# Kernel tuning notes

Measured on AMD Instinct MI355X. Metric: run time of the kernel, lower is better.

## Reference

```python
import jax, jax.numpy as jnp
import numpy as np
import math

D_MODEL = 256
NUM_SLOTS = 128
RANK = 32
STEPS = 6
VOCAB = 32000
SEQ = 512
BATCH = 8
LN_EPS = 1e-5


def setup_inputs() -> dict:
    key = jax.random.key(0)
    ks = jax.random.split(key, 16)
    std = 0.02
    inp = {
        "input_ids": jax.random.randint(ks[0], (BATCH, SEQ), 0, VOCAB),
        "attention_mask": jnp.ones((BATCH, SEQ), dtype=jnp.int32),
        "token_emb": jax.random.normal(ks[1], (VOCAB, D_MODEL), jnp.float32) * std,
        "pos_emb": jax.random.normal(ks[2], (SEQ, D_MODEL), jnp.float32) * std,
        "H": jax.random.normal(ks[3], (NUM_SLOTS, D_MODEL), jnp.float32) / math.sqrt(D_MODEL),
        "W_source": jax.random.normal(ks[4], (NUM_SLOTS, NUM_SLOTS, D_MODEL, RANK), jnp.float32) * std,
        "W_target": jax.random.normal(ks[5], (NUM_SLOTS, NUM_SLOTS, RANK, D_MODEL), jnp.float32) * std,
        "Wq_in": jax.random.normal(ks[6], (D_MODEL, D_MODEL), jnp.float32) / math.sqrt(D_MODEL),
        "Wk_slots": jax.random.normal(ks[7], (D_MODEL, D_MODEL), jnp.float32) / math.sqrt(D_MODEL),
        "Wv_in": jax.random.normal(ks[8], (D_MODEL, D_MODEL), jnp.float32) / math.sqrt(D_MODEL),
        "Wq_out": jax.random.normal(ks[9], (D_MODEL, D_MODEL), jnp.float32) / math.sqrt(D_MODEL),
        "Wk_fin": jax.random.normal(ks[10], (D_MODEL, D_MODEL), jnp.float32) / math.sqrt(D_MODEL),
        "Wv_fin": jax.random.normal(ks[11], (D_MODEL, D_MODEL), jnp.float32) / math.sqrt(D_MODEL),
        "W_out_proj": jax.random.normal(ks[12], (VOCAB, D_MODEL), jnp.float32) / math.sqrt(D_MODEL),
        "ln_scale": jnp.ones((STEPS, D_MODEL), jnp.float32),
        "ln_bias": jnp.zeros((STEPS, D_MODEL), jnp.float32),
    }
    return inp


def _layernorm(x, g, b):
    mu = jnp.mean(x, axis=-1, keepdims=True)
    var = jnp.var(x, axis=-1, keepdims=True)
    return (x - mu) / jnp.sqrt(var + LN_EPS) * g + b


def _forward(input_ids, attention_mask, token_emb, pos_emb, H, W_source, W_target,
             Wq_in, Wk_slots, Wv_in, Wq_out, Wk_fin, Wv_fin, W_out_proj, ln_scale, ln_bias):
    B, L = input_ids.shape
    scale = 1.0 / math.sqrt(D_MODEL)
    # embeddings (dropout is identity in eval)
    X = token_emb[input_ids] + pos_emb[jnp.arange(L)][None]  # (B,L,D)
    # compress: input tokens -> slots
    Q_in = X @ Wq_in.T                      # (B,L,D)
    K_sl = H @ Wk_slots.T                   # (S,D)
    V_in = X @ Wv_in.T                      # (B,L,D)
    A = jax.nn.softmax(Q_in @ K_sl.T * scale, axis=-1)  # (B,L,S)
    m = attention_mask.astype(A.dtype)[..., None]
    A = A * m
    A = A / (jnp.sum(A, axis=1, keepdims=True) + 1e-8)
    IR = jnp.einsum('bls,bld->bsd', A, V_in)            # (B,S,D)
    H_state = H[None] + IR                               # (B,S,D)

    off_diag = (1.0 - jnp.eye(NUM_SLOTS, dtype=H_state.dtype))  # (S,S)

    def step(h, lnp):
        g, b = lnp
        # bilinear slot-to-slot influence; contract directly, no (B,S,S,D) expand of h
        inter = jnp.einsum('bid,ijdr->bijr', h, W_source)        # (B,S,S,R)
        out = jnp.einsum('bijr,ijrd->bijd', inter, W_target)     # (B,S,S,D)
        infl = jnp.einsum('bijd,ij->bjd', out, off_diag)         # mask diag + sum over i
        h = _layernorm(h + jax.nn.relu(infl), g, b)
        return h, None

    H_state, _ = jax.lax.scan(step, H_state, (ln_scale, ln_bias))

    # expand: slots -> tokens
    Q_out = X @ Wq_out.T                   # (B,L,D)
    K_f = H_state @ Wk_fin.T               # (B,S,D)
    V_f = H_state @ Wv_fin.T               # (B,S,D)
    A2 = jax.nn.softmax(jnp.einsum('bld,bsd->bls', Q_out, K_f) * scale, axis=-1)
    Y = jnp.einsum('bls,bsd->bld', A2, V_f)
    logits = Y @ W_out_proj.T              # (B,L,V)
    return logits


def reference(input_ids, attention_mask, token_emb, pos_emb, H, W_source, W_target,
              Wq_in, Wk_slots, Wv_in, Wq_out, Wk_fin, Wv_fin, W_out_proj, ln_scale, ln_bias):
    return _forward(input_ids, attention_mask, token_emb, pos_emb, H, W_source, W_target,
                    Wq_in, Wk_slots, Wv_in, Wq_out, Wk_fin, Wv_fin, W_out_proj, ln_scale, ln_bias)
```

## Files before the change

kernel.cpp:

```cpp
#include <hip/hip_runtime.h>
#include <hip/hip_bf16.h>
#include <math.h>

#define D_MODEL 256
#define NUM_SLOTS 128
#define RANK 32
#define N_STEPS 6
#define VOCAB 32000
#define SEQ 512
#define BATCH 8
#define NTOK (BATCH*SEQ)
#define LN_EPS 1e-5f
#define SM_SCALE 0.0625f
#define IGROUPS 8
#define IPG (NUM_SLOTS/IGROUPS)

typedef __attribute__((ext_vector_type(8))) short bf16x8;
typedef __attribute__((ext_vector_type(8))) _Float16 f16x8;
typedef __attribute__((ext_vector_type(4))) float f32x4;

#define GLD_LDS16(g, l) __builtin_amdgcn_global_load_lds( \
    (const __attribute__((address_space(1))) unsigned int*)(g), \
    (__attribute__((address_space(3))) unsigned int*)(l), 16, 0, 0)

__device__ inline unsigned short f2bf(float x) {
    unsigned u = __float_as_uint(x);
    unsigned r = u + 0x7fff + ((u >> 16) & 1);
    return (unsigned short)(r >> 16);
}
__device__ inline float bf2f(unsigned short h) {
    return __uint_as_float(((unsigned)h) << 16);
}
__device__ inline unsigned pk2(float a, float b) {
    auto v = __builtin_amdgcn_cvt_pkrtz(a, b);
    union { decltype(v) x; unsigned u; } c;
    c.x = v;
    return c.u;
}
__device__ inline unsigned short f2h(float x) {
    union { _Float16 h; unsigned short u; } c;
    c.h = (_Float16)x;
    return c.u;
}
__device__ inline float h2f(unsigned short u) {
    union { unsigned short u; _Float16 h; } c;
    c.u = u;
    return (float)c.h;
}

__global__ __launch_bounds__(256) void k_embed(const int* __restrict__ ids,
        const float* __restrict__ tok, const float* __restrict__ pos,
        float* __restrict__ X) {
    int bl = blockIdx.x;
    int d  = threadIdx.x;
    int l  = bl % SEQ;
    int id = ids[bl];
    X[(size_t)bl*D_MODEL + d] = tok[(size_t)id*D_MODEL + d] + pos[l*D_MODEL + d];
}

__global__ __launch_bounds__(256) void k_gemm_nt(const float* __restrict__ A,
        const float* __restrict__ B, float* __restrict__ C, int M, int N, int K) {
    __shared__ float As[32][64];
    __shared__ float Bs[32][64];
    int bm = blockIdx.x * 64, bn = blockIdx.y * 64;
    int t = threadIdx.x;
    int tm = (t & 15) * 4, tn = (t >> 4) * 4;
    float acc[4][4] = {};
    for (int k0 = 0; k0 < K; k0 += 32) {
        #pragma unroll
        for (int r = 0; r < 8; ++r) {
            int idx = r*256 + t;
            int m = idx >> 5, k = idx & 31;
            As[k][m] = A[(size_t)(bm+m)*K + k0 + k];
        }
        #pragma unroll
        for (int r = 0; r < 8; ++r) {
            int idx = r*256 + t;
            int n = idx >> 5, k = idx & 31;
            Bs[k][n] = B[(size_t)(bn+n)*K + k0 + k];
        }
        __syncthreads();
        #pragma unroll
        for (int k = 0; k < 32; ++k) {
            float4 a4 = *(const float4*)&As[k][tm];
            float4 b4 = *(const float4*)&Bs[k][tn];
            float a[4] = {a4.x,a4.y,a4.z,a4.w};
            float b[4] = {b4.x,b4.y,b4.z,b4.w};
            #pragma unroll
            for (int i = 0; i < 4; ++i)
                #pragma unroll
                for (int jj = 0; jj < 4; ++jj)
                    acc[i][jj] += a[i]*b[jj];
        }
        __syncthreads();
    }
    #pragma unroll
    for (int i = 0; i < 4; ++i) {
        float4 v = make_float4(acc[i][0],acc[i][1],acc[i][2],acc[i][3]);
        *(float4*)&C[(size_t)(bm+tm+i)*N + bn+tn] = v;
    }
}

__global__ __launch_bounds__(256) void k_gemm3(const float* __restrict__ A,
        const float* __restrict__ B0, const float* __restrict__ B1,
        const float* __restrict__ B2, float* __restrict__ C0,
        float* __restrict__ C1, float* __restrict__ C2) {
    const int K = D_MODEL, N = D_MODEL;
    const float* B = blockIdx.z == 0 ? B0 : (blockIdx.z == 1 ? B1 : B2);
    float* C = blockIdx.z == 0 ? C0 : (blockIdx.z == 1 ? C1 : C2);
    __shared__ float As[32][64];
    __shared__ float Bs[32][64];
    int bm = blockIdx.x * 64, bn = blockIdx.y * 64;
    int t = threadIdx.x;
    int tm = (t & 15) * 4, tn = (t >> 4) * 4;
    float acc[4][4] = {};
    for (int k0 = 0; k0 < K; k0 += 32) {
        #pragma unroll
        for (int r = 0; r < 8; ++r) {
            int idx = r*256 + t;
            int m = idx >> 5, k = idx & 31;
            As[k][m] = A[(size_t)(bm+m)*K + k0 + k];
        }
        #pragma unroll
        for (int r = 0; r < 8; ++r) {
            int idx = r*256 + t;
            int n = idx >> 5, k = idx & 31;
            Bs[k][n] = B[(size_t)(bn+n)*K + k0 + k];
        }
        __syncthreads();
        #pragma unroll
        for (int k = 0; k < 32; ++k) {
            float4 a4 = *(const float4*)&As[k][tm];
            float4 b4 = *(const float4*)&Bs[k][tn];
            float a[4] = {a4.x,a4.y,a4.z,a4.w};
            float b[4] = {b4.x,b4.y,b4.z,b4.w};
            #pragma unroll
            for (int i = 0; i < 4; ++i)
                #pragma unroll
                for (int jj = 0; jj < 4; ++jj)
                    acc[i][jj] += a[i]*b[jj];
        }
        __syncthreads();
    }
    #pragma unroll
    for (int i = 0; i < 4; ++i) {
        float4 v = make_float4(acc[i][0],acc[i][1],acc[i][2],acc[i][3]);
        *(float4*)&C[(size_t)(bm+tm+i)*N + bn+tn] = v;
    }
}

__global__ __launch_bounds__(256) void k_split16(const float* __restrict__ in,
        unsigned short* __restrict__ o, int n4) {
    int i = blockIdx.x*256 + threadIdx.x;
    if (i >= n4) return;
    float4 v = ((const float4*)in)[i];
    ushort4 h;
    h.x = f2h(v.x); h.y = f2h(v.y); h.z = f2h(v.z); h.w = f2h(v.w);
    ((ushort4*)o)[i] = h;
}

__global__ __launch_bounds__(256) void k_logits(
        const unsigned short* __restrict__ Ahg, const unsigned short* __restrict__ Alg,
        const unsigned short* __restrict__ Bhg, float* __restrict__ C) {
    __shared__ short lds[3*128*64];
    short* Ah = lds;
    short* Al = lds + 8192;
    short* Bh = lds + 16384;
    int bm = blockIdx.x * 128, bn = blockIdx.y * 128;
    int t = threadIdx.x;
    int w = t >> 6, l = t & 63;
    int wr = w >> 1, wc = w & 1;
    int lr = l & 15, lk = l >> 4;
    f32x4 acc[4][4];
    #pragma unroll
    for (int mi = 0; mi < 4; ++mi)
        #pragma unroll
        for (int ni = 0; ni < 4; ++ni)
            acc[mi][ni] = (f32x4){0.f,0.f,0.f,0.f};

    for (int kc = 0; kc < 4; ++kc) {
        #pragma unroll
        for (int i = 0; i < 4; ++i) {
            int v = t + i*256;
            int row = v >> 3, cv = v & 7;
            int so = row*64 + ((cv ^ (row & 7)) << 3);
            size_t ga = (size_t)(bm+row)*256 + kc*64 + cv*8;
            size_t gb = (size_t)(bn+row)*256 + kc*64 + cv*8;
            *(bf16x8*)&Ah[so] = *(const bf16x8*)&Ahg[ga];
            *(bf16x8*)&Al[so] = *(const bf16x8*)&Alg[ga];
            *(bf16x8*)&Bh[so] = *(const bf16x8*)&Bhg[gb];
        }
        __syncthreads();
        #pragma unroll
        for (int s = 0; s < 2; ++s) {
            f16x8 ah[4], al[4], bh[4];
            #pragma unroll
            for (int mi = 0; mi < 4; ++mi) {
                int row = wr*64 + mi*16 + lr;
                int off = row*64 + ((((s<<2)+lk) ^ (row&7)) << 3);
                ah[mi] = *(f16x8*)&Ah[off];
                al[mi] = *(f16x8*)&Al[off];
            }
            #pragma unroll
            for (int ni = 0; ni < 4; ++ni) {
                int row = wc*64 + ni*16 + lr;
                int off = row*64 + ((((s<<2)+lk) ^ (row&7)) << 3);
                bh[ni] = *(f16x8*)&Bh[off];
            }
            #pragma unroll
            for (int mi = 0; mi < 4; ++mi)
                #pragma unroll
                for (int ni = 0; ni < 4; ++ni) {
                    acc[mi][ni] = __builtin_amdgcn_mfma_f32_16x16x32_f16(ah[mi], bh[ni], acc[mi][ni], 0, 0, 0);
                    acc[mi][ni] = __builtin_amdgcn_mfma_f32_16x16x32_f16(al[mi], bh[ni], acc[mi][ni], 0, 0, 0);
                }
        }
        __syncthreads();
    }
    #pragma unroll
    for (int mi = 0; mi < 4; ++mi)
        #pragma unroll
        for (int ni = 0; ni < 4; ++ni) {
            int col = bn + wc*64 + ni*16 + lr;
            #pragma unroll
            for (int r = 0; r < 4; ++r) {
                int row = bm + wr*64 + mi*16 + lk*4 + r;
                C[(size_t)row*VOCAB + col] = acc[mi][ni][r];
            }
        }
}

__global__ __launch_bounds__(128) void k_softmax_mask(float* __restrict__ A,
        const int* __restrict__ mask) {
    int row = blockIdx.x;
    int s = threadIdx.x;
    __shared__ float red[128];
    float v = A[(size_t)row*NUM_SLOTS + s] * SM_SCALE;
    red[s] = v; __syncthreads();
    for (int o = 64; o > 0; o >>= 1) { if (s < o) red[s] = fmaxf(red[s], red[s+o]); __syncthreads(); }
    float mx = red[0]; __syncthreads();
    float e = expf(v - mx);
    red[s] = e; __syncthreads();
    for (int o = 64; o > 0; o >>= 1) { if (s < o) red[s] += red[s+o]; __syncthreads(); }
    float sum = red[0];
    float m = (float)mask[row];
    A[(size_t)row*NUM_SLOTS + s] = e / sum * m;
}

__global__ __launch_bounds__(128) void k_colsum(const float* __restrict__ A,
        float* __restrict__ csp) {
    int b = blockIdx.x; int ch = blockIdx.y; int s = threadIdx.x;
    const float* Ab = A + ((size_t)b*SEQ + ch*64)*NUM_SLOTS + s;
    float a0 = 0.f, a1 = 0.f, a2 = 0.f, a3 = 0.f;
    #pragma unroll
    for (int l = 0; l < 64; l += 4) {
        a0 += Ab[(size_t)(l+0)*NUM_SLOTS];
        a1 += Ab[(size_t)(l+1)*NUM_SLOTS];
        a2 += Ab[(size_t)(l+2)*NUM_SLOTS];
        a3 += Ab[(size_t)(l+3)*NUM_SLOTS];
    }
    csp[(b*8 + ch)*NUM_SLOTS + s] = (a0+a1) + (a2+a3);
}

__global__ __launch_bounds__(256) void k_ir(const float* __restrict__ A,
        const float* __restrict__ V, const float* __restrict__ H,
        const float* __restrict__ csp, float* __restrict__ Hs,
        unsigned short* __restrict__ Hs16) {
    int bs = blockIdx.x; int b = bs >> 7; int s = bs & 127;
    int d = threadIdx.x;
    float sum = 1e-8f;
    #pragma unroll
    for (int p = 0; p < 8; ++p) sum += csp[(b*8 + p)*NUM_SLOTS + s];
    float inv = 1.0f / sum;
    const float* Ab = A + (size_t)b*SEQ*NUM_SLOTS + s;
    const float* Vb = V + (size_t)b*SEQ*D_MODEL + d;
    float a0 = 0.f, a1 = 0.f, a2 = 0.f, a3 = 0.f;
    for (int l = 0; l < SEQ; l += 4) {
        a0 += Ab[(size_t)(l+0)*NUM_SLOTS] * Vb[(size_t)(l+0)*D_MODEL];
        a1 += Ab[(size_t)(l+1)*NUM_SLOTS] * Vb[(size_t)(l+1)*D_MODEL];
        a2 += Ab[(size_t)(l+2)*NUM_SLOTS] * Vb[(size_t)(l+2)*D_MODEL];
        a3 += Ab[(size_t)(l+3)*NUM_SLOTS] * Vb[(size_t)(l+3)*D_MODEL];
    }
    float acc = (a0+a1) + (a2+a3);
    float v = H[s*D_MODEL + d] + acc * inv;
    Hs[(size_t)bs*D_MODEL + d] = v;
    Hs16[(size_t)bs*D_MODEL + d] = f2h(v);
}

__global__ __launch_bounds__(256) void k_convert_s(const float* __restrict__ Ws,
        unsigned short* __restrict__ WF) {
    int i = blockIdx.x, j = blockIdx.y, hf = blockIdx.z;
    int t = threadIdx.x;
    __shared__ float lds[128*33];
    size_t sBase = ((size_t)i*128 + j)*8192;
    size_t pOut = ((size_t)j*128 + i)*16384;
    const float4* s4 = (const float4*)(Ws + sBase) + hf*1024;
    #pragma unroll
    for (int p = 0; p < 4; ++p) {
        int f4 = p*256 + t;
        float4 v = s4[f4];
        *(float4*)&lds[(f4 >> 3)*33 + 4*(f4 & 7)] = v;
    }
    __syncthreads();
    bool diag = (i == j);
    #pragma unroll
    for (int q = 0; q < 2; ++q) {
        int cl = q*256 + t;
        int ksl = cl >> 7, mt = (cl >> 6) & 1, l = cl & 63;
        int g = l >> 4, c = l & 15;
        union { f16x8 v; } o;
        #pragma unroll
        for (int e = 0; e < 8; ++e) {
            float f = diag ? 0.f : lds[(ksl*32 + g*8 + e)*33 + mt*16 + c];
            o.v[e] = (_Float16)f;
        }
        *(f16x8*)(WF + pOut + (size_t)hf*4096 + (size_t)cl*8) = o.v;
    }
}

__global__ __launch_bounds__(256) void k_convert_t(const float* __restrict__ Wt,
        unsigned short* __restrict__ WF) {
    int i = blockIdx.x, j = blockIdx.y, hf = blockIdx.z;
    int t = threadIdx.x;
    __shared__ float lds[32*133];
    size_t sBase = ((size_t)i*128 + j)*8192;
    size_t pOut = ((size_t)j*128 + i)*16384;
    const float4* s4 = (const float4*)(Wt + sBase);
    #pragma unroll
    for (int p = 0; p < 4; ++p) {
        int idx = p*256 + t;
        int r = idx >> 5, c4 = idx & 31;
        float4 v = s4[r*64 + hf*32 + c4];
        *(float4*)&lds[r*133 + c4*4] = v;
    }
    __syncthreads();
    #pragma unroll
    for (int q = 0; q < 2; ++q) {
        int cl = q*256 + t;
        int ntl = cl >> 6, l = cl & 63;
        int g = l >> 4, c = l & 15;
        union { f16x8 v; } o;
        #pragma unroll
        for (int e = 0; e < 8; ++e)
            o.v[e] = (_Float16)lds[(g*8 + e)*133 + ntl*16 + c];
        *(f16x8*)(WF + pOut + 8192 + (size_t)hf*4096 + (size_t)cl*8) = o.v;
    }
}

__global__ __launch_bounds__(256, 4) void k_pairs_mfma(const unsigned short* __restrict__ h16,
        const unsigned short* __restrict__ WF, float* __restrict__ part) {
    __shared__ unsigned short lds[2*10240];
    int j = blockIdx.x, g = blockIdx.y;
    int t = threadIdx.x, w = t >> 6, l = t & 63;
    int lg = l >> 4, c = l & 15;
    const unsigned short* pbase = WF + ((size_t)j*128 + g*16)*16384;

    {
        const unsigned short* src = pbase;
        #pragma unroll
        for (int q = 0; q < 4; ++q)
            GLD_LDS16(src + (size_t)(q*256 + t)*8, &lds[(q*256 + t)*8]);
        const unsigned short* hsrc = h16 + ((size_t)(t&7)*NUM_SLOTS + g*16)*D_MODEL + (t>>3)*8;
        GLD_LDS16(hsrc, &lds[8192 + t*8]);
    }
    __builtin_amdgcn_sched_barrier(0);
    f16x8 bqn[4];
    #pragma unroll
    for (int nt = 0; nt < 4; ++nt)
        bqn[nt] = *(const f16x8*)(pbase + 8192 + (size_t)((w*4+nt)*64 + l)*8);
    __builtin_amdgcn_sched_barrier(0);

    f32x4 acc[4];
    #pragma unroll
    for (int nt = 0; nt < 4; ++nt) acc[nt] = (f32x4){0.f,0.f,0.f,0.f};
    f16x8 hzero;
    #pragma unroll
    for (int e = 0; e < 8; ++e) hzero[e] = (_Float16)0.f;

    #pragma unroll 2
    for (int ii = 0; ii < 16; ++ii) {
        int cur = ii & 1;
        asm volatile("s_waitcnt vmcnt(4) lgkmcnt(0)" ::: "memory");
        __builtin_amdgcn_s_barrier();
        __builtin_amdgcn_sched_barrier(0);
        if (ii < 15) {
            const unsigned short* src = pbase + (size_t)(ii+1)*16384;
            unsigned short* dst = &lds[(cur^1)*10240];
            #pragma unroll
            for (int q = 0; q < 4; ++q)
                GLD_LDS16(src + (size_t)(q*256 + t)*8, dst + (size_t)(q*256 + t)*8);
            const unsigned short* hsrc = h16 + ((size_t)(t&7)*NUM_SLOTS + (g*16+ii+1))*D_MODEL + (t>>3)*8;
            GLD_LDS16(hsrc, dst + 8192 + (size_t)t*8);
        }
        __builtin_amdgcn_sched_barrier(0);
        f16x8 bq[4];
        #pragma unroll
        for (int nt = 0; nt < 4; ++nt) bq[nt] = bqn[nt];
        if (ii < 15) {
            const unsigned short* bp = pbase + (size_t)(ii+1)*16384 + 8192;
            #pragma unroll
            for (int nt = 0; nt < 4; ++nt)
                bqn[nt] = *(const f16x8*)(bp + (size_t)((w*4+nt)*64 + l)*8);
        }
        const unsigned short* buf = &lds[cur*10240];
        f32x4 d1[2];
        d1[0] = (f32x4){0.f,0.f,0.f,0.f};
        d1[1] = (f32x4){0.f,0.f,0.f,0.f};
        #pragma unroll
        for (int ks = 0; ks < 8; ++ks) {
            f16x8 a0 = *(const f16x8*)(buf + (size_t)((ks*2+0)*64 + l)*8);
            f16x8 a1 = *(const f16x8*)(buf + (size_t)((ks*2+1)*64 + l)*8);
            f16x8 hv = *(const f16x8*)(buf + 8192 + (size_t)(((ks*4+lg)*8 + (c&7)))*8);
            f16x8 hb = (c < 8) ? hv : hzero;
            d1[0] = __builtin_amdgcn_mfma_f32_16x16x32_f16(a0, hb, d1[0], 0, 0, 0);
            d1[1] = __builtin_amdgcn_mfma_f32_16x16x32_f16(a1, hb, d1[1], 0, 0, 0);
        }
        unsigned q0 = pk2(d1[0][0], d1[0][1]);
        unsigned q1 = pk2(d1[0][2], d1[0][3]);
        unsigned s0 = pk2(d1[1][0], d1[1][1]);
        unsigned s1 = pk2(d1[1][2], d1[1][3]);
        int srcLo = 32*(lg & 1) + c;
        int srcHi = srcLo + 16;
        unsigned a0s = (unsigned)__shfl((int)q0, srcLo, 64);
        unsigned a1s = (unsigned)__shfl((int)q1, srcLo, 64);
        unsigned a2s = (unsigned)__shfl((int)q0, srcHi, 64);
        unsigned a3s = (unsigned)__shfl((int)q1, srcHi, 64);
        unsigned b0s = (unsigned)__shfl((int)s0, srcLo, 64);
        unsigned b1s = (unsigned)__shfl((int)s1, srcLo, 64);
        unsigned b2s = (unsigned)__shfl((int)s0, srcHi, 64);
        unsigned b3s = (unsigned)__shfl((int)s1, srcHi, 64);
        bool himt = ((lg >> 1) & 1);
        union { unsigned u[4]; f16x8 v; } A2u;
        A2u.u[0] = himt ? b0s : a0s;
        A2u.u[1] = himt ? b1s : a1s;
        A2u.u[2] = himt ? b2s : a2s;
        A2u.u[3] = himt ? b3s : a3s;
        #pragma unroll
        for (int nt = 0; nt < 4; ++nt)
            acc[nt] = __builtin_amdgcn_mfma_f32_16x16x32_f16(A2u.v, bq[nt], acc[nt], 0, 0, 0);
    }
    if (lg < 2) {
        #pragma unroll
        for (int nt = 0; nt < 4; ++nt) {
            int d = (w*4 + nt)*16 + c;
            #pragma unroll
            for (int r = 0; r < 4; ++r) {
                int b = lg*4 + r;
                part[(((size_t)g*BATCH + b)*NUM_SLOTS + j)*D_MODEL + d] = acc[nt][r];
            }
        }
    }
}

__global__ __launch_bounds__(256) void k_pairs(const float* __restrict__ h,
        const float* __restrict__ Ws, const float* __restrict__ Wt,
        float* __restrict__ part) {
    int j = blockIdx.x;
    int g = blockIdx.y;
    int t = threadIdx.x;
    __shared__ float sh_h[BATCH][D_MODEL];
    __shared__ float sh_inter[BATCH][RANK];
    float acc[BATCH];
    #pragma unroll
    for (int b = 0; b < BATCH; ++b) acc[b] = 0.f;
    int tb = t >> 5, tr = t & 31;
    for (int ii = 0; ii < IPG; ++ii) {
        int i = g*IPG + ii;
        if (i == j) continue;
        #pragma unroll
        for (int b = 0; b < BATCH; ++b)
            sh_h[b][t] = h[((size_t)b*NUM_SLOTS + i)*D_MODEL + t];
        __syncthreads();
        const float* ws = Ws + ((size_t)i*NUM_SLOTS + j)*(D_MODEL*RANK);
        float accA = 0.f;
        #pragma unroll 8
        for (int d = 0; d < D_MODEL; ++d)
            accA += sh_h[tb][d] * ws[(size_t)d*RANK + tr];
        sh_inter[tb][tr] = accA;
        __syncthreads();
        const float* wt = Wt + ((size_t)i*NUM_SLOTS + j)*(RANK*D_MODEL);
        #pragma unroll 8
        for (int r = 0; r < RANK; ++r) {
            float w = wt[(size_t)r*D_MODEL + t];
            #pragma unroll
            for (int b = 0; b < BATCH; ++b) acc[b] += sh_inter[b][r] * w;
        }
        __syncthreads();
    }
    #pragma unroll
    for (int b = 0; b < BATCH; ++b)
        part[(((size_t)g*BATCH + b)*NUM_SLOTS + j)*D_MODEL + t] = acc[b];
}

__global__ __launch_bounds__(256) void k_ln(float* __restrict__ h,
        unsigned short* __restrict__ h16, const float* __restrict__ part,
        const float* __restrict__ gma, const float* __restrict__ bta) {
    int bj = blockIdx.x;
    int t = threadIdx.x;
    int b = bj >> 7, j = bj & 127;
    __shared__ float red[256];
    float v = 0.f;
    #pragma unroll
    for (int g = 0; g < IGROUPS; ++g)
        v += part[(((size_t)g*BATCH + b)*NUM_SLOTS + j)*D_MODEL + t];
    float x = h[(size_t)bj*D_MODEL + t] + fmaxf(v, 0.f);
    red[t] = x; __syncthreads();
    for (int o = 128; o > 0; o >>= 1) { if (t < o) red[t] += red[t+o]; __syncthreads(); }
    float mu = red[0] * (1.0f/D_MODEL); __syncthreads();
    float dx = x - mu;
    red[t] = dx*dx; __syncthreads();
    for (int o = 128; o > 0; o >>= 1) { if (t < o) red[t] += red[t+o]; __syncthreads(); }
    float var = red[0] * (1.0f/D_MODEL);
    float outv = dx * rsqrtf(var + LN_EPS) * gma[t] + bta[t];
    h[(size_t)bj*D_MODEL + t] = outv;
    h16[(size_t)bj*D_MODEL + t] = f2h(outv);
}

__global__ __launch_bounds__(128) void k_attn2(const float* __restrict__ Q,
        const float* __restrict__ Kf, float* __restrict__ A2) {
    int bl = blockIdx.x; int b = bl / SEQ;
    int s = threadIdx.x;
    __shared__ float q[D_MODEL];
    __shared__ float red[128];
    q[s]       = Q[(size_t)bl*D_MODEL + s];
    q[s + 128] = Q[(size_t)bl*D_MODEL + s + 128];
    __syncthreads();
    const float* kf = Kf + ((size_t)b*NUM_SLOTS + s)*D_MODEL;
    float acc = 0.f;
    #pragma unroll 8
    for (int d = 0; d < D_MODEL; ++d) acc += q[d]*kf[d];
    acc *= SM_SCALE;
    red[s] = acc; __syncthreads();
    for (int o = 64; o > 0; o >>= 1) { if (s < o) red[s] = fmaxf(red[s], red[s+o]); __syncthreads(); }
    float mx = red[0]; __syncthreads();
    float e = expf(acc - mx);
    red[s] = e; __syncthreads();
    for (int o = 64; o > 0; o >>= 1) { if (s < o) red[s] += red[s+o]; __syncthreads(); }
    A2[(size_t)bl*NUM_SLOTS + s] = e / red[0];
}

__global__ __launch_bounds__(256) void k_y(const float* __restrict__ A2,
        const float* __restrict__ Vf, unsigned short* __restrict__ Yh,
        unsigned short* __restrict__ Yl) {
    int bl = blockIdx.x; int b = bl / SEQ;
    int d = threadIdx.x;
    const float* a = A2 + (size_t)bl*NUM_SLOTS;
    const float* v = Vf + (size_t)b*NUM_SLOTS*D_MODEL + d;
    float acc = 0.f;
    #pragma unroll 4
    for (int s = 0; s < NUM_SLOTS; ++s) acc += a[s]*v[(size_t)s*D_MODEL];
    unsigned short yh = f2h(acc);
    Yh[(size_t)bl*D_MODEL + d] = yh;
    Yl[(size_t)bl*D_MODEL + d] = f2h(acc - h2f(yh));
}

extern "C" void kernel_launch(void* const* d_in, const int* in_sizes, int n_in,
                              void* d_out, int out_size, void* d_ws, size_t ws_size,
                              hipStream_t stream) {
    const int*   ids    = (const int*)d_in[0];
    const int*   amask  = (const int*)d_in[1];
    const float* tok    = (const float*)d_in[2];
    const float* pos    = (const float*)d_in[3];
    const float* Hin    = (const float*)d_in[4];
    const float* Ws     = (const float*)d_in[5];
    const float* Wt     = (const float*)d_in[6];
    const float* Wq_in  = (const float*)d_in[7];
    const float* Wk_sl  = (const float*)d_in[8];
    const float* Wv_in  = (const float*)d_in[9];
    const float* Wq_out = (const float*)d_in[10];
    const float* Wk_fin = (const float*)d_in[11];
    const float* Wv_fin = (const float*)d_in[12];
    const float* Wop    = (const float*)d_in[13];
    const float* lnsc   = (const float*)d_in[14];
    const float* lnbs   = (const float*)d_in[15];
    float* out = (float*)d_out;

    const size_t WF_USH = (size_t)16384 * 16384;
    const size_t F32_FLOATS = 18600000ULL;
    const bool useF16 = ws_size >= WF_USH*2 + F32_FLOATS*4 + 256;

    unsigned short* WF = (unsigned short*)d_ws;
    float* ws = useF16 ? (float*)(WF + WF_USH) : (float*)d_ws;

    float* X    = ws;
    float* Qin  = X    + (size_t)NTOK*D_MODEL;
    float* Vin  = Qin  + (size_t)NTOK*D_MODEL;
    float* Ksl  = Vin  + (size_t)NTOK*D_MODEL;
    float* Asc  = Ksl  + (size_t)NUM_SLOTS*D_MODEL;
    float* csp  = Asc  + (size_t)NTOK*NUM_SLOTS;
    float* Hst  = csp  + (size_t)BATCH*8*NUM_SLOTS;
    float* part = Hst  + (size_t)BATCH*NUM_SLOTS*D_MODEL;
    float* Qout = part + (size_t)IGROUPS*BATCH*NUM_SLOTS*D_MODEL;
    float* Kf   = Qout + (size_t)NTOK*D_MODEL;
    float* Vf   = Kf   + (size_t)BATCH*NUM_SLOTS*D_MODEL;
    float* A2   = Vf   + (size_t)BATCH*NUM_SLOTS*D_MODEL;
    float* Yb   = A2   + (size_t)NTOK*NUM_SLOTS;
    unsigned short* Yh = (unsigned short*)(Yb + (size_t)NTOK*D_MODEL);
    unsigned short* Yl = Yh + (size_t)NTOK*D_MODEL;
    unsigned short* Wf16 = Yl + (size_t)NTOK*D_MODEL;
    unsigned short* Hst16 = Wf16 + (size_t)VOCAB*D_MODEL;

    if (useF16) {
        k_convert_s<<<dim3(128, 128, 2), 256, 0, stream>>>(Ws, WF);
        k_convert_t<<<dim3(128, 128, 2), 256, 0, stream>>>(Wt, WF);
    }
    k_split16<<<(VOCAB*D_MODEL/4 + 255)/256, 256, 0, stream>>>(Wop, Wf16, VOCAB*D_MODEL/4);

    k_embed<<<NTOK, 256, 0, stream>>>(ids, tok, pos, X);
    k_gemm3<<<dim3(NTOK/64, 4, 3), 256, 0, stream>>>(X, Wq_in, Wv_in, Wq_out, Qin, Vin, Qout);
    k_gemm_nt<<<dim3(2, 4), 256, 0, stream>>>(Hin, Wk_sl, Ksl, NUM_SLOTS, D_MODEL, D_MODEL);
    k_gemm_nt<<<dim3(NTOK/64, 2), 256, 0, stream>>>(Qin, Ksl, Asc, NTOK, NUM_SLOTS, D_MODEL);
    k_softmax_mask<<<NTOK, 128, 0, stream>>>(Asc, amask);
    k_colsum<<<dim3(BATCH, 8), 128, 0, stream>>>(Asc, csp);
    k_ir<<<BATCH*NUM_SLOTS, 256, 0, stream>>>(Asc, Vin, Hin, csp, Hst, Hst16);
    for (int st = 0; st < N_STEPS; ++st) {
        if (useF16)
            k_pairs_mfma<<<dim3(NUM_SLOTS, IGROUPS), 256, 0, stream>>>(Hst16, WF, part);
        else
            k_pairs<<<dim3(NUM_SLOTS, IGROUPS), 256, 0, stream>>>(Hst, Ws, Wt, part);
        k_ln<<<BATCH*NUM_SLOTS, 256, 0, stream>>>(Hst, Hst16, part, lnsc + st*D_MODEL, lnbs + st*D_MODEL);
    }
    k_gemm_nt<<<dim3(BATCH*NUM_SLOTS/64, 4), 256, 0, stream>>>(Hst, Wk_fin, Kf, BATCH*NUM_SLOTS, D_MODEL, D_MODEL);
    k_gemm_nt<<<dim3(BATCH*NUM_SLOTS/64, 4), 256, 0, stream>>>(Hst, Wv_fin, Vf, BATCH*NUM_SLOTS, D_MODEL, D_MODEL);
    k_attn2<<<NTOK, 128, 0, stream>>>(Qout, Kf, A2);
    k_y<<<NTOK, 256, 0, stream>>>(A2, Vf, Yh, Yl);
    k_logits<<<dim3(NTOK/128, VOCAB/128), 256, 0, stream>>>(Yh, Yl, Wf16, out);
}
```

Before: 1.513 ms.

## Fuse final attention kernels, merge conversions, use direct global-to-LDS loads in logits

```diff
diff --git a/kernel.cpp b/kernel.cpp
--- a/kernel.cpp
+++ b/kernel.cpp
@@ -149,6 +149,53 @@
     }
 }
 
+__global__ __launch_bounds__(256) void k_kfvf(const float* __restrict__ A,
+        const float* __restrict__ B0, const float* __restrict__ B1,
+        float* __restrict__ C0, float* __restrict__ C1) {
+    const int K = D_MODEL, N = D_MODEL;
+    const float* B = blockIdx.z == 0 ? B0 : B1;
+    float* C = blockIdx.z == 0 ? C0 : C1;
+    __shared__ float As[32][64];
+    __shared__ float Bs[32][64];
+    int bm = blockIdx.x * 64, bn = blockIdx.y * 64;
+    int t = threadIdx.x;
+    int tm = (t & 15) * 4, tn = (t >> 4) * 4;
+    float acc[4][4] = {};
+    for (int k0 = 0; k0 < K; k0 += 32) {
+        #pragma unroll
+        for (int r = 0; r < 8; ++r) {
+            int idx = r*256 + t;
+            int m = idx >> 5, k = idx & 31;
+            As[k][m] = A[(size_t)(bm+m)*K + k0 + k];
+        }
+        #pragma unroll
+        for (int r = 0; r < 8; ++r) {
+            int idx = r*256 + t;
+            int n = idx >> 5, k = idx & 31;
+            Bs[k][n] = B[(size_t)(bn+n)*K + k0 + k];
+        }
+        __syncthreads();
+        #pragma unroll
+        for (int k = 0; k < 32; ++k) {
+            float4 a4 = *(const float4*)&As[k][tm];
+            float4 b4 = *(const float4*)&Bs[k][tn];
+            float a[4] = {a4.x,a4.y,a4.z,a4.w};
+            float b[4] = {b4.x,b4.y,b4.z,b4.w};
+            #pragma unroll
+            for (int i = 0; i < 4; ++i)
+                #pragma unroll
+                for (int jj = 0; jj < 4; ++jj)
+                    acc[i][jj] += a[i]*b[jj];
+        }
+        __syncthreads();
+    }
+    #pragma unroll
+    for (int i = 0; i < 4; ++i) {
+        float4 v = make_float4(acc[i][0],acc[i][1],acc[i][2],acc[i][3]);
+        *(float4*)&C[(size_t)(bm+tm+i)*N + bn+tn] = v;
+    }
+}
+
 __global__ __launch_bounds__(256) void k_split16(const float* __restrict__ in,
         unsigned short* __restrict__ o, int n4) {
     int i = blockIdx.x*256 + threadIdx.x;
@@ -162,10 +209,7 @@
 __global__ __launch_bounds__(256) void k_logits(
         const unsigned short* __restrict__ Ahg, const unsigned short* __restrict__ Alg,
         const unsigned short* __restrict__ Bhg, float* __restrict__ C) {
-    __shared__ short lds[3*128*64];
-    short* Ah = lds;
-    short* Al = lds + 8192;
-    short* Bh = lds + 16384;
+    __shared__ unsigned short lds[3*8192];
     int bm = blockIdx.x * 128, bn = blockIdx.y * 128;
     int t = threadIdx.x;
     int w = t >> 6, l = t & 63;
@@ -179,16 +223,16 @@
             acc[mi][ni] = (f32x4){0.f,0.f,0.f,0.f};
 
     for (int kc = 0; kc < 4; ++kc) {
+        if (kc) __syncthreads();
         #pragma unroll
         for (int i = 0; i < 4; ++i) {
-            int v = t + i*256;
-            int row = v >> 3, cv = v & 7;
-            int so = row*64 + ((cv ^ (row & 7)) << 3);
-            size_t ga = (size_t)(bm+row)*256 + kc*64 + cv*8;
-            size_t gb = (size_t)(bn+row)*256 + kc*64 + cv*8;
-            *(bf16x8*)&Ah[so] = *(const bf16x8*)&Ahg[ga];
-            *(bf16x8*)&Al[so] = *(const bf16x8*)&Alg[ga];
-            *(bf16x8*)&Bh[so] = *(const bf16x8*)&Bhg[gb];
+            int c = t + i*256;
+            int row = c >> 3, c8 = c & 7;
+            size_t ga = (size_t)(bm+row)*256 + kc*64 + c8*8;
+            size_t gb = (size_t)(bn+row)*256 + kc*64 + c8*8;
+            GLD_LDS16(Ahg + ga, &lds[c*8]);
+            GLD_LDS16(Alg + ga, &lds[8192 + c*8]);
+            GLD_LDS16(Bhg + gb, &lds[16384 + c*8]);
         }
         __syncthreads();
         #pragma unroll
@@ -196,16 +240,14 @@
             f16x8 ah[4], al[4], bh[4];
             #pragma unroll
             for (int mi = 0; mi < 4; ++mi) {
-                int row = wr*64 + mi*16 + lr;
-                int off = row*64 + ((((s<<2)+lk) ^ (row&7)) << 3);
-                ah[mi] = *(f16x8*)&Ah[off];
-                al[mi] = *(f16x8*)&Al[off];
+                int off = (wr*64 + mi*16 + lr)*64 + s*32 + lk*8;
+                ah[mi] = *(const f16x8*)&lds[off];
+                al[mi] = *(const f16x8*)&lds[8192 + off];
             }
             #pragma unroll
             for (int ni = 0; ni < 4; ++ni) {
-                int row = wc*64 + ni*16 + lr;
-                int off = row*64 + ((((s<<2)+lk) ^ (row&7)) << 3);
-                bh[ni] = *(f16x8*)&Bh[off];
+                int off = (wc*64 + ni*16 + lr)*64 + s*32 + lk*8;
+                bh[ni] = *(const f16x8*)&lds[16384 + off];
             }
             #pragma unroll
             for (int mi = 0; mi < 4; ++mi)
@@ -215,7 +257,6 @@
                     acc[mi][ni] = __builtin_amdgcn_mfma_f32_16x16x32_f16(al[mi], bh[ni], acc[mi][ni], 0, 0, 0);
                 }
         }
-        __syncthreads();
     }
     #pragma unroll
     for (int mi = 0; mi < 4; ++mi)
@@ -287,63 +328,59 @@
     Hs16[(size_t)bs*D_MODEL + d] = f2h(v);
 }
 
-__global__ __launch_bounds__(256) void k_convert_s(const float* __restrict__ Ws,
-        unsigned short* __restrict__ WF) {
-    int i = blockIdx.x, j = blockIdx.y, hf = blockIdx.z;
-    int t = threadIdx.x;
-    __shared__ float lds[128*33];
+__global__ __launch_bounds__(256) void k_convert(const float* __restrict__ Ws,
+        const float* __restrict__ Wt, unsigned short* __restrict__ WF) {
+    int i = blockIdx.x, j = blockIdx.y, z = blockIdx.z;
+    int t = threadIdx.x;
+    __shared__ float lds[4352];
     size_t sBase = ((size_t)i*128 + j)*8192;
     size_t pOut = ((size_t)j*128 + i)*16384;
-    const float4* s4 = (const float4*)(Ws + sBase) + hf*1024;
-    #pragma unroll
-    for (int p = 0; p < 4; ++p) {
-        int f4 = p*256 + t;
-        float4 v = s4[f4];
-        *(float4*)&lds[(f4 >> 3)*33 + 4*(f4 & 7)] = v;
-    }
-    __syncthreads();
-    bool diag = (i == j);
-    #pragma unroll
-    for (int q = 0; q < 2; ++q) {
-        int cl = q*256 + t;
-        int ksl = cl >> 7, mt = (cl >> 6) & 1, l = cl & 63;
-        int g = l >> 4, c = l & 15;
-        union { f16x8 v; } o;
-        #pragma unroll
-        for (int e = 0; e < 8; ++e) {
-            float f = diag ? 0.f : lds[(ksl*32 + g*8 + e)*33 + mt*16 + c];
-            o.v[e] = (_Float16)f;
-        }
-        *(f16x8*)(WF + pOut + (size_t)hf*4096 + (size_t)cl*8) = o.v;
-    }
-}
-
-__global__ __launch_bounds__(256) void k_convert_t(const float* __restrict__ Wt,
-        unsigned short* __restrict__ WF) {
-    int i = blockIdx.x, j = blockIdx.y, hf = blockIdx.z;
-    int t = threadIdx.x;
-    __shared__ float lds[32*133];
-    size_t sBase = ((size_t)i*128 + j)*8192;
-    size_t pOut = ((size_t)j*128 + i)*16384;
-    const float4* s4 = (const float4*)(Wt + sBase);
-    #pragma unroll
-    for (int p = 0; p < 4; ++p) {
-        int idx = p*256 + t;
-        int r = idx >> 5, c4 = idx & 31;
-        float4 v = s4[r*64 + hf*32 + c4];
-        *(float4*)&lds[r*133 + c4*4] = v;
-    }
-    __syncthreads();
-    #pragma unroll
-    for (int q = 0; q < 2; ++q) {
-        int cl = q*256 + t;
-        int ntl = cl >> 6, l = cl & 63;
-        int g = l >> 4, c = l & 15;
-        union { f16x8 v; } o;
-        #pragma unroll
-        for (int e = 0; e < 8; ++e)
-            o.v[e] = (_Float16)lds[(g*8 + e)*133 + ntl*16 + c];
-        *(f16x8*)(WF + pOut + 8192 + (size_t)hf*4096 + (size_t)cl*8) = o.v;
+    if (z < 2) {
+        int hf = z;
+        const float4* s4 = (const float4*)(Ws + sBase) + hf*1024;
+        #pragma unroll
+        for (int p = 0; p < 4; ++p) {
+            int f4 = p*256 + t;
+            float4 v = s4[f4];
+            *(float4*)&lds[(f4 >> 3)*33 + 4*(f4 & 7)] = v;
+        }
+        __syncthreads();
+        bool diag = (i == j);
+        #pragma unroll
+        for (int q = 0; q < 2; ++q) {
+            int cl = q*256 + t;
+            int ksl = cl >> 7, mt = (cl >> 6) & 1, l = cl & 63;
+            int g = l >> 4, c = l & 15;
+            union { f16x8 v; } o;
+            #pragma unroll
+            for (int e = 0; e < 8; ++e) {
+                float f = diag ? 0.f : lds[(ksl*32 + g*8 + e)*33 + mt*16 + c];
+                o.v[e] = (_Float16)f;
+            }
+            *(f16x8*)(WF + pOut + (size_t)hf*4096 + (size_t)cl*8) = o.v;
+        }
+    } else {
+        int hf = z - 2;
+        const float4* s4 = (const float4*)(Wt + sBase);
+        #pragma unroll
+        for (int p = 0; p < 4; ++p) {
+            int idx = p*256 + t;
+            int r = idx >> 5, c4 = idx & 31;
+            float4 v = s4[r*64 + hf*32 + c4];
+            *(float4*)&lds[r*133 + c4*4] = v;
+        }
+        __syncthreads();
+        #pragma unroll
+        for (int q = 0; q < 2; ++q) {
+            int cl = q*256 + t;
+            int ntl = cl >> 6, l = cl & 63;
+            int g = l >> 4, c = l & 15;
+            union { f16x8 v; } o;
+            #pragma unroll
+            for (int e = 0; e < 8; ++e)
+                o.v[e] = (_Float16)lds[(g*8 + e)*133 + ntl*16 + c];
+            *(f16x8*)(WF + pOut + 8192 + (size_t)hf*4096 + (size_t)cl*8) = o.v;
+        }
     }
 }
 
@@ -516,42 +553,47 @@
     h16[(size_t)bj*D_MODEL + t] = f2h(outv);
 }
 
-__global__ __launch_bounds__(128) void k_attn2(const float* __restrict__ Q,
-        const float* __restrict__ Kf, float* __restrict__ A2) {
+__global__ __launch_bounds__(256) void k_attn2y(const float* __restrict__ Q,
+        const float* __restrict__ Kf, const float* __restrict__ Vf,
+        unsigned short* __restrict__ Yh, unsigned short* __restrict__ Yl) {
     int bl = blockIdx.x; int b = bl / SEQ;
-    int s = threadIdx.x;
+    int t = threadIdx.x;
     __shared__ float q[D_MODEL];
+    __shared__ float prt[2][128];
+    __shared__ float a[128];
     __shared__ float red[128];
-    q[s]       = Q[(size_t)bl*D_MODEL + s];
-    q[s + 128] = Q[(size_t)bl*D_MODEL + s + 128];
+    q[t] = Q[(size_t)bl*D_MODEL + t];
     __syncthreads();
-    const float* kf = Kf + ((size_t)b*NUM_SLOTS + s)*D_MODEL;
-    float acc = 0.f;
+    int s = t & 127, hf = t >> 7;
+    const float* kf = Kf + ((size_t)b*NUM_SLOTS + s)*D_MODEL + hf*128;
+    float accp = 0.f;
     #pragma unroll 8
-    for (int d = 0; d < D_MODEL; ++d) acc += q[d]*kf[d];
-    acc *= SM_SCALE;
-    red[s] = acc; __syncthreads();
-    for (int o = 64; o > 0; o >>= 1) { if (s < o) red[s] = fmaxf(red[s], red[s+o]); __syncthreads(); }
+    for (int d = 0; d < 128; ++d) accp += q[hf*128 + d]*kf[d];
+    prt[hf][s] = accp;
+    __syncthreads();
+    float v = 0.f;
+    if (t < 128) { v = (prt[0][t] + prt[1][t]) * SM_SCALE; red[t] = v; }
+    __syncthreads();
+    for (int o = 64; o > 0; o >>= 1) { if (t < o) red[t] = fmaxf(red[t], red[t+o]); __syncthreads(); }
     float mx = red[0]; __syncthreads();
-    float e = expf(acc - mx);
-    red[s] = e; __syncthreads();
-    for (int o = 64; o > 0; o >>= 1) { if (s < o) red[s] += red[s+o]; __syncthreads(); }
-    A2[(size_t)bl*NUM_SLOTS + s] = e / red[0];
-}
-
-__global__ __launch_bounds__(256) void k_y(const float* __restrict__ A2,
-        const float* __restrict__ Vf, unsigned short* __restrict__ Yh,
-        unsigned short* __restrict__ Yl) {
-    int bl = blockIdx.x; int b = bl / SEQ;
-    int d = threadIdx.x;
-    const float* a = A2 + (size_t)bl*NUM_SLOTS;
-    const float* v = Vf + (size_t)b*NUM_SLOTS*D_MODEL + d;
-    float acc = 0.f;
-    #pragma unroll 4
-    for (int s = 0; s < NUM_SLOTS; ++s) acc += a[s]*v[(size_t)s*D_MODEL];
-    unsigned short yh = f2h(acc);
-    Yh[(size_t)bl*D_MODEL + d] = yh;
-    Yl[(size_t)bl*D_MODEL + d] = f2h(acc - h2f(yh));
+    if (t < 128) { float e = expf(v - mx); a[t] = e; red[t] = e; }
+    __syncthreads();
+    for (int o = 64; o > 0; o >>= 1) { if (t < o) red[t] += red[t+o]; __syncthreads(); }
+    float inv = 1.0f / red[0];
+    __syncthreads();
+    const float* vf = Vf + (size_t)b*NUM_SLOTS*D_MODEL + t;
+    float y0 = 0.f, y1 = 0.f, y2 = 0.f, y3 = 0.f;
+    #pragma unroll
+    for (int s2 = 0; s2 < NUM_SLOTS; s2 += 4) {
+        y0 += a[s2+0]*vf[(size_t)(s2+0)*D_MODEL];
+        y1 += a[s2+1]*vf[(size_t)(s2+1)*D_MODEL];
+        y2 += a[s2+2]*vf[(size_t)(s2+2)*D_MODEL];
+        y3 += a[s2+3]*vf[(size_t)(s2+3)*D_MODEL];
+    }
+    float y = ((y0+y1) + (y2+y3)) * inv;
+    unsigned short yh = f2h(y);
+    Yh[(size_t)bl*D_MODEL + t] = yh;
+    Yl[(size_t)bl*D_MODEL + t] = f2h(y - h2f(yh));
 }
 
 extern "C" void kernel_launch(void* const* d_in, const int* in_sizes, int n_in,
@@ -600,10 +642,8 @@
     unsigned short* Wf16 = Yl + (size_t)NTOK*D_MODEL;
     unsigned short* Hst16 = Wf16 + (size_t)VOCAB*D_MODEL;
 
-    if (useF16) {
-        k_convert_s<<<dim3(128, 128, 2), 256, 0, stream>>>(Ws, WF);
-        k_convert_t<<<dim3(128, 128, 2), 256, 0, stream>>>(Wt, WF);
-    }
+    if (useF16)
+        k_convert<<<dim3(128, 128, 4), 256, 0, stream>>>(Ws, Wt, WF);
     k_split16<<<(VOCAB*D_MODEL/4 + 255)/256, 256, 0, stream>>>(Wop, Wf16, VOCAB*D_MODEL/4);
 
     k_embed<<<NTOK, 256, 0, stream>>>(ids, tok, pos, X);
@@ -620,9 +660,7 @@
             k_pairs<<<dim3(NUM_SLOTS, IGROUPS), 256, 0, stream>>>(Hst, Ws, Wt, part);
         k_ln<<<BATCH*NUM_SLOTS, 256, 0, stream>>>(Hst, Hst16, part, lnsc + st*D_MODEL, lnbs + st*D_MODEL);
     }
-    k_gemm_nt<<<dim3(BATCH*NUM_SLOTS/64, 4), 256, 0, stream>>>(Hst, Wk_fin, Kf, BATCH*NUM_SLOTS, D_MODEL, D_MODEL);
-    k_gemm_nt<<<dim3(BATCH*NUM_SLOTS/64, 4), 256, 0, stream>>>(Hst, Wv_fin, Vf, BATCH*NUM_SLOTS, D_MODEL, D_MODEL);
-    k_attn2<<<NTOK, 128, 0, stream>>>(Qout, Kf, A2);
-    k_y<<<NTOK, 256, 0, stream>>>(A2, Vf, Yh, Yl);
+    k_kfvf<<<dim3(BATCH*NUM_SLOTS/64, 4, 2), 256, 0, stream>>>(Hst, Wk_fin, Wv_fin, Kf, Vf);
+    k_attn2y<<<NTOK, 256, 0, stream>>>(Qout, Kf, Vf, Yh, Yl);
     k_logits<<<dim3(NTOK/128, VOCAB/128), 256, 0, stream>>>(Yh, Yl, Wf16, out);
 }
```

New measurement: 1.471 ms. 1.03x faster.
